# Kernel tuning notes

Hardware: AMD Instinct MI355X
Metric: run time of the kernel (lower is better)

The kernel has to match this reference:

```python
import jax, jax.numpy as jnp
import numpy as np

EMBED = 768
HEADS = 12
HEAD_DIM = EMBED // HEADS
FFN = 4 * EMBED
EPS = 1e-5


def setup_inputs() -> dict:
    key = jax.random.key(0)
    ks = jax.random.split(key, 12)
    s = 0.02
    inp = {
        'x': jax.random.normal(ks[0], (1, 4096, EMBED), dtype=jnp.float32),
        'Wq': jax.random.normal(ks[1], (EMBED, EMBED), dtype=jnp.float32) * s,
        'bq': jnp.zeros((EMBED,), jnp.float32),
        'Wk': jax.random.normal(ks[2], (EMBED, EMBED), dtype=jnp.float32) * s,
        'bk': jnp.zeros((EMBED,), jnp.float32),
        'Wv': jax.random.normal(ks[3], (EMBED, EMBED), dtype=jnp.float32) * s,
        'bv': jnp.zeros((EMBED,), jnp.float32),
        'Wo': jax.random.normal(ks[4], (EMBED, EMBED), dtype=jnp.float32) * s,
        'bo': jnp.zeros((EMBED,), jnp.float32),
        'ln1_g': jnp.ones((EMBED,), jnp.float32),
        'ln1_b': jnp.zeros((EMBED,), jnp.float32),
        'W1': jax.random.normal(ks[5], (EMBED, FFN), dtype=jnp.float32) * s,
        'b1': jnp.zeros((FFN,), jnp.float32),
        'W2': jax.random.normal(ks[6], (FFN, EMBED), dtype=jnp.float32) * s,
        'b2': jnp.zeros((EMBED,), jnp.float32),
        'ln2_g': jnp.ones((EMBED,), jnp.float32),
        'ln2_b': jnp.zeros((EMBED,), jnp.float32),
    }
    return inp


def _layernorm(x, g, b):
    mu = jnp.mean(x, axis=-1, keepdims=True)
    var = jnp.mean(jnp.square(x - mu), axis=-1, keepdims=True)
    return (x - mu) * jax.lax.rsqrt(var + EPS) * g + b


def reference(x, Wq, bq, Wk, bk, Wv, bv, Wo, bo, ln1_g, ln1_b, W1, b1, W2, b2, ln2_g, ln2_b):
    B, S, D = x.shape
    # QKV projections -> [B, H, S, d]
    def split_heads(t):
        return t.reshape(B, S, HEADS, HEAD_DIM).transpose(0, 2, 1, 3)
    q = split_heads(x @ Wq + bq)
    k = split_heads(x @ Wk + bk)
    v = split_heads(x @ Wv + bv)
    scores = jnp.einsum('bhqd,bhkd->bhqk', q, k) / np.sqrt(HEAD_DIM).astype(np.float32)
    attn = jax.nn.softmax(scores, axis=-1)
    ctx = jnp.einsum('bhqk,bhkd->bhqd', attn, v)
    ctx = ctx.transpose(0, 2, 1, 3).reshape(B, S, D)
    attn_out = ctx @ Wo + bo
    h = _layernorm(x + attn_out, ln1_g, ln1_b)
    ffn = jax.nn.gelu(h @ W1 + b1, approximate=False) @ W2 + b2
    return _layernorm(h + ffn, ln2_g, ln2_b)
```

## Files before the change

kernel.cpp:

```cpp
#include <hip/hip_runtime.h>
#include <hip/hip_bf16.h>

typedef __attribute__((ext_vector_type(8))) short s16x8;
typedef __attribute__((ext_vector_type(4))) int   i32x4;
typedef __attribute__((ext_vector_type(4))) float f32x4;
typedef __attribute__((ext_vector_type(8))) __bf16 bf16x8;

__device__ __forceinline__ short f2bf(float f) {
  unsigned u = __builtin_bit_cast(unsigned, f);
  u = (u + 0x7FFFu + ((u >> 16) & 1u)) >> 16;
  return (short)u;
}
__device__ __forceinline__ float bf2f(short s) {
  unsigned u = ((unsigned)(unsigned short)s) << 16;
  return __builtin_bit_cast(float, u);
}
__device__ __forceinline__ f32x4 mfma16(s16x8 a, s16x8 b, f32x4 c) {
  return __builtin_amdgcn_mfma_f32_16x16x32_bf16(
      __builtin_bit_cast(bf16x8, a), __builtin_bit_cast(bf16x8, b), c, 0, 0, 0);
}
__device__ __forceinline__ void gload16(const void* g, void* l) {
  __builtin_amdgcn_global_load_lds(
      (const __attribute__((address_space(1))) void*)g,
      (__attribute__((address_space(3))) void*)l, 16, 0, 0);
}

__global__ __launch_bounds__(256) void convert_x_kernel(const float* __restrict__ src,
                                                        short* __restrict__ dst, int n8) {
  int i = blockIdx.x * 256 + threadIdx.x;
  if (i >= n8) return;
  float4 v0 = ((const float4*)src)[i * 2];
  float4 v1 = ((const float4*)src)[i * 2 + 1];
  s16x8 o;
  o[0] = f2bf(v0.x); o[1] = f2bf(v0.y); o[2] = f2bf(v0.z); o[3] = f2bf(v0.w);
  o[4] = f2bf(v1.x); o[5] = f2bf(v1.y); o[6] = f2bf(v1.z); o[7] = f2bf(v1.w);
  *(s16x8*)&dst[i * 8] = o;
}

__global__ __launch_bounds__(256) void bconcat_kernel(const float* __restrict__ bq,
                                                      const float* __restrict__ bk,
                                                      const float* __restrict__ bv,
                                                      float* __restrict__ out) {
  int i = blockIdx.x * 256 + threadIdx.x;
  if (i < 2304) out[i] = i < 768 ? bq[i] : (i < 1536 ? bk[i - 768] : bv[i - 1536]);
}

__global__ __launch_bounds__(256) void wconv_kernel(const float* __restrict__ src,
                                                    short* __restrict__ dst, int K, int N) {
  __shared__ float t[32][33];
  int n0 = blockIdx.x * 32, k0 = blockIdx.y * 32;
  int tx = threadIdx.x & 31, ty = threadIdx.x >> 5;
#pragma unroll
  for (int r = 0; r < 4; ++r) t[ty + r * 8][tx] = src[(long)(k0 + ty + r * 8) * N + n0 + tx];
  __syncthreads();
#pragma unroll
  for (int r = 0; r < 4; ++r)
    dst[(long)(n0 + ty + r * 8) * K + k0 + tx] = f2bf(t[tx][ty + r * 8]);
}

__global__ __launch_bounds__(256) void vtrans_kernel(const short* __restrict__ qkv,
                                                     short* __restrict__ vt) {
  __shared__ short t[32][34];
  int c0 = blockIdx.x * 32, s0 = blockIdx.y * 32;
  int tx = threadIdx.x & 31, ty = threadIdx.x >> 5;
#pragma unroll
  for (int r = 0; r < 4; ++r)
    t[ty + r * 8][tx] = qkv[(long)(s0 + ty + r * 8) * 2304 + 1536 + c0 + tx];
  __syncthreads();
#pragma unroll
  for (int r = 0; r < 4; ++r)
    vt[(long)(c0 + ty + r * 8) * 4096 + s0 + tx] = t[tx][ty + r * 8];
}

template <int OUT_MODE>
__global__ __launch_bounds__(256) void gemm_kernel(const short* __restrict__ A,
                                                   const short* __restrict__ Bt,
                                                   const float* __restrict__ bias,
                                                   void* __restrict__ Cout,
                                                   int M, int N, int Kfull, int Ksub) {
  __shared__ short As[2][128 * 32];
  __shared__ short Bs[2][128 * 32];
  const int tid = threadIdx.x;
  const int wave = tid >> 6, lane = tid & 63;
  const int lr = lane & 15, lg = lane >> 4;
  const int wm = wave >> 1, wn = wave & 1;
  const int bm = blockIdx.x, bn = blockIdx.y;
  const long koff = (long)blockIdx.z * Ksub;

  f32x4 acc[4][4] = {};

  const int r0 = tid >> 2;
  const int cc = (tid & 3) * 8;
  const short* Ag0 = A + (long)(bm * 128 + r0) * Kfull + koff + cc;
  const short* Ag1 = Ag0 + (long)64 * Kfull;
  const short* Bg0 = Bt + (long)(bn * 128 + r0) * Kfull + koff + cc;
  const short* Bg1 = Bg0 + (long)64 * Kfull;

  auto STAGE = [&](int buf, int k0) {
    gload16(Ag0 + k0, &As[buf][tid * 8]);
    gload16(Ag1 + k0, &As[buf][64 * 32 + tid * 8]);
    gload16(Bg0 + k0, &Bs[buf][tid * 8]);
    gload16(Bg1 + k0, &Bs[buf][64 * 32 + tid * 8]);
  };
  auto COMPUTE = [&](int buf) {
    s16x8 af[4], bfr[4];
#pragma unroll
    for (int m = 0; m < 4; ++m) {
      int row = wm * 64 + m * 16 + lr;
      af[m] = *(const s16x8*)&As[buf][row * 32 + lg * 8];
    }
#pragma unroll
    for (int n = 0; n < 4; ++n) {
      int row = wn * 64 + n * 16 + lr;
      bfr[n] = *(const s16x8*)&Bs[buf][row * 32 + lg * 8];
    }
#pragma unroll
    for (int m = 0; m < 4; ++m)
#pragma unroll
      for (int n = 0; n < 4; ++n)
        acc[m][n] = mfma16(af[m], bfr[n], acc[m][n]);
  };

  const int nt = Ksub >> 5;
  STAGE(0, 0);
  int cur = 0;
  for (int t = 0; t < nt - 1; ++t) {
    STAGE(cur ^ 1, (t + 1) * 32);
    asm volatile("s_waitcnt vmcnt(4)" ::: "memory");
    __builtin_amdgcn_s_barrier();
    __builtin_amdgcn_sched_barrier(0);
    COMPUTE(cur);
    __builtin_amdgcn_s_barrier();
    cur ^= 1;
  }
  asm volatile("s_waitcnt vmcnt(0)" ::: "memory");
  __builtin_amdgcn_s_barrier();
  __builtin_amdgcn_sched_barrier(0);
  COMPUTE(cur);

  const int gr0 = bm * 128 + wm * 64 + lg * 4;
  const int gc0 = bn * 128 + wn * 64 + lr;
  float* outF = (float*)Cout + (long)blockIdx.z * M * N;
#pragma unroll
  for (int n = 0; n < 4; ++n) {
    int col = gc0 + n * 16;
    float bb = (blockIdx.z == 0) ? bias[col] : 0.f;
#pragma unroll
    for (int m = 0; m < 4; ++m) {
#pragma unroll
      for (int j = 0; j < 4; ++j) {
        int row = gr0 + m * 16 + j;
        float v = acc[m][n][j] + bb;
        if (OUT_MODE == 2) v = 0.5f * v * (1.0f + erff(v * 0.70710678118f));
        if (OUT_MODE == 1) outF[(long)row * N + col] = v;
        else ((short*)Cout)[(long)row * N + col] = f2bf(v);
      }
    }
  }
}

__global__ __launch_bounds__(256) void flash_kernel(const short* __restrict__ qkv,
                                                    const short* __restrict__ vt,
                                                    float* __restrict__ Opart,
                                                    float* __restrict__ Lpart) {
  __shared__ short Kt[2][64 * 64];
  __shared__ short Vs[2][64 * 64];
  __shared__ short Ps[128 * 72];
  const int tid = threadIdx.x;
  const int wave = tid >> 6, lane = tid & 63;
  const int lr = lane & 15, lg = lane >> 4;
  const int h = blockIdx.y, qb = blockIdx.x, sp = blockIdx.z;
  const int qc = h * 64;
  const int hc = 768 + h * 64;
  const int vr = h * 64;
  const float QSCALE = 0.125f * 1.44269504088896f;

  auto STAGEKV = [&](int buf, int s0) {
#pragma unroll
    for (int i = 0; i < 2; ++i) {
      int c = tid + i * 256;
      int row = c >> 3;
      int ch = (c & 7) ^ (row & 7);
      gload16(&qkv[(long)(s0 + row) * 2304 + hc + ch * 8], &Kt[buf][c * 8]);
      gload16(&vt[(long)(vr + row) * 4096 + s0 + ch * 8], &Vs[buf][c * 8]);
    }
  };

#pragma unroll
  for (int i = 0; i < 4; ++i) {
    int c = tid + i * 256;
    int row = c >> 3, cq = (c & 7) * 8;
    *(i32x4*)&Ps[row * 72 + cq] =
        *(const i32x4*)&qkv[(long)(qb * 128 + row) * 2304 + qc + cq];
  }
  STAGEKV(0, sp * 2048);
  __syncthreads();
  s16x8 qf[2][2];
#pragma unroll
  for (int m = 0; m < 2; ++m)
#pragma unroll
    for (int ks = 0; ks < 2; ++ks) {
      int row = wave * 32 + m * 16 + lr;
      s16x8 v = *(const s16x8*)&Ps[row * 72 + ks * 32 + lg * 8];
#pragma unroll
      for (int e = 0; e < 8; ++e) {
        __bf16 b = (__bf16)(bf2f(v[e]) * QSCALE);
        v[e] = (short)__builtin_bit_cast(unsigned short, b);
      }
      qf[m][ks] = v;
    }

  float l_part[8];
#pragma unroll
  for (int i = 0; i < 8; ++i) l_part[i] = 0.f;
  f32x4 oacc[2][4] = {};

  int cur = 0;
  for (int it = 0; it < 32; ++it) {
    if (it != 31) {
      STAGEKV(cur ^ 1, sp * 2048 + (it + 1) * 64);
      asm volatile("s_waitcnt vmcnt(4)" ::: "memory");
    } else {
      asm volatile("s_waitcnt vmcnt(0)" ::: "memory");
    }
    __builtin_amdgcn_s_barrier();
    __builtin_amdgcn_sched_barrier(0);

    f32x4 sacc[2][4] = {};
#pragma unroll
    for (int ks = 0; ks < 2; ++ks) {
      s16x8 kf[4];
#pragma unroll
      for (int n = 0; n < 4; ++n) {
        int row = n * 16 + lr;
        int chk = (ks * 4 + lg) ^ (lr & 7);
        kf[n] = *(const s16x8*)&Kt[cur][row * 64 + chk * 8];
      }
      __builtin_amdgcn_s_setprio(1);
#pragma unroll
      for (int m = 0; m < 2; ++m)
#pragma unroll
        for (int n = 0; n < 4; ++n)
          sacc[m][n] = mfma16(qf[m][ks], kf[n], sacc[m][n]);
      __builtin_amdgcn_s_setprio(0);
    }
#pragma unroll
    for (int m = 0; m < 2; ++m) {
#pragma unroll
      for (int j = 0; j < 4; ++j) {
        const int prow = wave * 32 + m * 16 + lg * 4 + j;
        float rs = 0.f;
#pragma unroll
        for (int n = 0; n < 4; ++n) {
          float p = __builtin_amdgcn_exp2f(sacc[m][n][j]);
          rs += p;
          ((__bf16*)Ps)[prow * 72 + n * 16 + lr] = (__bf16)p;
        }
        l_part[m * 4 + j] += rs;
      }
    }
#pragma unroll
    for (int ks = 0; ks < 2; ++ks) {
      s16x8 pf[2], vf[4];
#pragma unroll
      for (int m = 0; m < 2; ++m) {
        int row = wave * 32 + m * 16 + lr;
        pf[m] = *(const s16x8*)&Ps[row * 72 + ks * 32 + lg * 8];
      }
#pragma unroll
      for (int n = 0; n < 4; ++n) {
        int row = n * 16 + lr;
        int chk = (ks * 4 + lg) ^ (lr & 7);
        vf[n] = *(const s16x8*)&Vs[cur][row * 64 + chk * 8];
      }
      __builtin_amdgcn_s_setprio(1);
#pragma unroll
      for (int m = 0; m < 2; ++m)
#pragma unroll
        for (int n = 0; n < 4; ++n)
          oacc[m][n] = mfma16(pf[m], vf[n], oacc[m][n]);
      __builtin_amdgcn_s_setprio(0);
    }
    __builtin_amdgcn_s_barrier();
    cur ^= 1;
  }

  const long pbase = ((long)(h * 32 + qb) * 2 + sp) * 128;
#pragma unroll
  for (int m = 0; m < 2; ++m)
#pragma unroll
    for (int j = 0; j < 4; ++j) {
      float l = l_part[m * 4 + j];
      l += __shfl_xor(l, 1);
      l += __shfl_xor(l, 2);
      l += __shfl_xor(l, 4);
      l += __shfl_xor(l, 8);
      if (lr == 0) Lpart[pbase + wave * 32 + m * 16 + lg * 4 + j] = l;
    }
#pragma unroll
  for (int m = 0; m < 2; ++m)
#pragma unroll
    for (int n = 0; n < 4; ++n)
#pragma unroll
      for (int j = 0; j < 4; ++j) {
        int row = wave * 32 + m * 16 + lg * 4 + j;
        Opart[(pbase + row) * 64 + n * 16 + lr] = oacc[m][n][j];
      }
}

__global__ __launch_bounds__(256) void combine_kernel(const float* __restrict__ Opart,
                                                      const float* __restrict__ Lpart,
                                                      short* __restrict__ ctx) {
  const int row = blockIdx.x;
  const int col = blockIdx.y * 256 + threadIdx.x;
  const int h = col >> 6, c = col & 63;
  const int qb = row >> 7, r = row & 127;
  const long p0 = ((long)(h * 32 + qb) * 2) * 128 + r;
  const long p1 = p0 + 128;
  float l = Lpart[p0] + Lpart[p1];
  float o = Opart[p0 * 64 + c] + Opart[p1 * 64 + c];
  ctx[(long)row * 768 + col] = f2bf(o / l);
}

__global__ __launch_bounds__(256) void ln_kernel(const float* __restrict__ a,
                                                 const float* __restrict__ b,
                                                 const float* __restrict__ c,
                                                 const float* __restrict__ g,
                                                 const float* __restrict__ be,
                                                 float* __restrict__ of,
                                                 short* __restrict__ ob) {
  const int row = blockIdx.x;
  const int tid = threadIdx.x;
  const long base = (long)row * 768;
  float v[3];
  float s1 = 0.f, s2 = 0.f;
#pragma unroll
  for (int kk = 0; kk < 3; ++kk) {
    int i = tid + kk * 256;
    float x = a[base + i] + b[base + i] + c[base + i];
    v[kk] = x;
    s1 += x;
    s2 += x * x;
  }
#pragma unroll
  for (int off = 1; off < 64; off <<= 1) {
    s1 += __shfl_xor(s1, off);
    s2 += __shfl_xor(s2, off);
  }
  __shared__ float ws1[4], ws2[4];
  int wave = tid >> 6;
  if ((tid & 63) == 0) { ws1[wave] = s1; ws2[wave] = s2; }
  __syncthreads();
  s1 = ws1[0] + ws1[1] + ws1[2] + ws1[3];
  s2 = ws2[0] + ws2[1] + ws2[2] + ws2[3];
  float mean = s1 * (1.f / 768.f);
  float var = s2 * (1.f / 768.f) - mean * mean;
  float rstd = rsqrtf(var + 1e-5f);
#pragma unroll
  for (int kk = 0; kk < 3; ++kk) {
    int i = tid + kk * 256;
    float o = (v[kk] - mean) * rstd * g[i] + be[i];
    if (of) of[base + i] = o;
    if (ob) ob[base + i] = f2bf(o);
  }
}

extern "C" void kernel_launch(void* const* d_in, const int* in_sizes, int n_in,
                              void* d_out, int out_size, void* d_ws, size_t ws_size,
                              hipStream_t stream) {
  const float* x   = (const float*)d_in[0];
  const float* Wq  = (const float*)d_in[1];
  const float* bq  = (const float*)d_in[2];
  const float* Wk  = (const float*)d_in[3];
  const float* bk  = (const float*)d_in[4];
  const float* Wv  = (const float*)d_in[5];
  const float* bv  = (const float*)d_in[6];
  const float* Wo  = (const float*)d_in[7];
  const float* bo  = (const float*)d_in[8];
  const float* g1  = (const float*)d_in[9];
  const float* be1 = (const float*)d_in[10];
  const float* W1  = (const float*)d_in[11];
  const float* b1  = (const float*)d_in[12];
  const float* W2  = (const float*)d_in[13];
  const float* b2  = (const float*)d_in[14];
  const float* g2  = (const float*)d_in[15];
  const float* be2 = (const float*)d_in[16];

  char* ws = (char*)d_ws;
  size_t off = 0;
  auto alloc = [&](size_t bytes) {
    char* p = ws + off;
    off += (bytes + 255) & ~(size_t)255;
    return p;
  };
  short* xb     = (short*)alloc(4096ul * 768 * 2);
  short* wqkv_t = (short*)alloc(2304ul * 768 * 2);
  short* wo_t   = (short*)alloc(768ul * 768 * 2);
  short* w1_t   = (short*)alloc(3072ul * 768 * 2);
  short* w2_t   = (short*)alloc(768ul * 3072 * 2);
  float* bqkv   = (float*)alloc(2304ul * 4);
  short* qkv    = (short*)alloc(4096ul * 2304 * 2);
  short* vt     = (short*)alloc(768ul * 4096 * 2);
  short* ctx    = (short*)alloc(4096ul * 768 * 2);
  float* attn_o = (float*)alloc(4096ul * 768 * 4);
  short* h_b    = (short*)alloc(4096ul * 768 * 2);
  float* h_f    = (float*)alloc(4096ul * 768 * 4);
  short* f1     = (short*)alloc(4096ul * 3072 * 2);
  float* Opart  = (float*)f1;
  float* Lpart  = (float*)attn_o;
  float* attn_p = (float*)qkv;
  float* ffn_p  = (float*)qkv;

  convert_x_kernel<<<1536, 256, 0, stream>>>(x, xb, 4096 * 768 / 8);
  bconcat_kernel<<<9, 256, 0, stream>>>(bq, bk, bv, bqkv);
  wconv_kernel<<<dim3(24, 24), 256, 0, stream>>>(Wq, wqkv_t, 768, 768);
  wconv_kernel<<<dim3(24, 24), 256, 0, stream>>>(Wk, wqkv_t + 768 * 768, 768, 768);
  wconv_kernel<<<dim3(24, 24), 256, 0, stream>>>(Wv, wqkv_t + 2 * 768 * 768, 768, 768);
  wconv_kernel<<<dim3(24, 24), 256, 0, stream>>>(Wo, wo_t, 768, 768);
  wconv_kernel<<<dim3(96, 24), 256, 0, stream>>>(W1, w1_t, 768, 3072);
  wconv_kernel<<<dim3(24, 96), 256, 0, stream>>>(W2, w2_t, 3072, 768);

  gemm_kernel<0><<<dim3(32, 18), 256, 0, stream>>>(xb, wqkv_t, bqkv, qkv, 4096, 2304, 768, 768);
  vtrans_kernel<<<dim3(24, 128), 256, 0, stream>>>(qkv, vt);
  flash_kernel<<<dim3(32, 12, 2), 256, 0, stream>>>(qkv, vt, Opart, Lpart);
  combine_kernel<<<dim3(4096, 3), 256, 0, stream>>>(Opart, Lpart, ctx);
  gemm_kernel<1><<<dim3(32, 6, 2), 256, 0, stream>>>(ctx, wo_t, bo, attn_p, 4096, 768, 768, 384);
  ln_kernel<<<4096, 256, 0, stream>>>(x, attn_p, attn_p + 4096ul * 768, g1, be1, h_f, h_b);
  gemm_kernel<2><<<dim3(32, 24), 256, 0, stream>>>(h_b, w1_t, b1, f1, 4096, 3072, 768, 768);
  gemm_kernel<1><<<dim3(32, 6, 2), 256, 0, stream>>>(f1, w2_t, b2, ffn_p, 4096, 768, 3072, 1536);
  ln_kernel<<<4096, 256, 0, stream>>>(h_f, ffn_p, ffn_p + 4096ul * 768, g2, be2, (float*)d_out, nullptr);
}
```

Measured before the change: 264.0 us.

## Prefetch K/V tiles through registers into single LDS buffer and remap block order

The flash kernel's double-buffered direct global-to-LDS loads are replaced by register prefetch. The next K/V tile is loaded into registers while the current tile is computed, then written into a single swizzled LDS buffer at the top of each iteration. Halving the K/V shared memory is meant to improve occupancy. Block indices are also remapped so that consecutive hardware blocks are spread across heads and splits, which is meant to improve L2/XCD locality. The cost is extra VGPRs and a store-to-LDS step on the critical path at the start of each iteration.

```diff
diff --git a/kernel.cpp b/kernel.cpp
--- a/kernel.cpp
+++ b/kernel.cpp
@@ -163,28 +163,42 @@
                                                     const short* __restrict__ vt,
                                                     float* __restrict__ Opart,
                                                     float* __restrict__ Lpart) {
-  __shared__ short Kt[2][64 * 64];
-  __shared__ short Vs[2][64 * 64];
+  __shared__ short Kt[64 * 64];
+  __shared__ short Vs[64 * 64];
   __shared__ short Ps[128 * 72];
   const int tid = threadIdx.x;
   const int wave = tid >> 6, lane = tid & 63;
   const int lr = lane & 15, lg = lane >> 4;
-  const int h = blockIdx.y, qb = blockIdx.x, sp = blockIdx.z;
+  const int lb = blockIdx.x + 32 * blockIdx.y + 384 * blockIdx.z;
+  const int nlb = (lb & 7) * 96 + (lb >> 3);
+  const int qb = nlb & 31;
+  const int h = (nlb >> 5) % 12;
+  const int sp = nlb / 384;
   const int qc = h * 64;
   const int hc = 768 + h * 64;
   const int vr = h * 64;
   const float QSCALE = 0.125f * 1.44269504088896f;
 
-  auto STAGEKV = [&](int buf, int s0) {
+  i32x4 kr[2], vrg[2];
+  auto LOADREGS = [&](int s0) {
 #pragma unroll
     for (int i = 0; i < 2; ++i) {
-      int c = tid + i * 256;
-      int row = c >> 3;
-      int ch = (c & 7) ^ (row & 7);
-      gload16(&qkv[(long)(s0 + row) * 2304 + hc + ch * 8], &Kt[buf][c * 8]);
-      gload16(&vt[(long)(vr + row) * 4096 + s0 + ch * 8], &Vs[buf][c * 8]);
+      int c = tid + i * 256, row = c >> 3, ch = c & 7;
+      kr[i] = *(const i32x4*)&qkv[(long)(s0 + row) * 2304 + hc + ch * 8];
+      vrg[i] = *(const i32x4*)&vt[(long)(vr + row) * 4096 + s0 + ch * 8];
     }
   };
+  auto WRITELDS = [&]() {
+#pragma unroll
+    for (int i = 0; i < 2; ++i) {
+      int c = tid + i * 256, row = c >> 3, ch = c & 7;
+      int sc = ch ^ (row & 7);
+      *(i32x4*)&Kt[row * 64 + sc * 8] = kr[i];
+      *(i32x4*)&Vs[row * 64 + sc * 8] = vrg[i];
+    }
+  };
+
+  LOADREGS(sp * 2048);
 
 #pragma unroll
   for (int i = 0; i < 4; ++i) {
@@ -193,7 +207,6 @@
     *(i32x4*)&Ps[row * 72 + cq] =
         *(const i32x4*)&qkv[(long)(qb * 128 + row) * 2304 + qc + cq];
   }
-  STAGEKV(0, sp * 2048);
   __syncthreads();
   s16x8 qf[2][2];
 #pragma unroll
@@ -215,14 +228,10 @@
   for (int i = 0; i < 8; ++i) l_part[i] = 0.f;
   f32x4 oacc[2][4] = {};
 
-  int cur = 0;
   for (int it = 0; it < 32; ++it) {
-    if (it != 31) {
-      STAGEKV(cur ^ 1, sp * 2048 + (it + 1) * 64);
-      asm volatile("s_waitcnt vmcnt(4)" ::: "memory");
-    } else {
-      asm volatile("s_waitcnt vmcnt(0)" ::: "memory");
-    }
+    WRITELDS();
+    if (it != 31) LOADREGS(sp * 2048 + (it + 1) * 64);
+    asm volatile("s_waitcnt lgkmcnt(0)" ::: "memory");
     __builtin_amdgcn_s_barrier();
     __builtin_amdgcn_sched_barrier(0);
 
@@ -234,7 +243,7 @@
       for (int n = 0; n < 4; ++n) {
         int row = n * 16 + lr;
         int chk = (ks * 4 + lg) ^ (lr & 7);
-        kf[n] = *(const s16x8*)&Kt[cur][row * 64 + chk * 8];
+        kf[n] = *(const s16x8*)&Kt[row * 64 + chk * 8];
       }
       __builtin_amdgcn_s_setprio(1);
 #pragma unroll
@@ -271,7 +280,7 @@
       for (int n = 0; n < 4; ++n) {
         int row = n * 16 + lr;
         int chk = (ks * 4 + lg) ^ (lr & 7);
-        vf[n] = *(const s16x8*)&Vs[cur][row * 64 + chk * 8];
+        vf[n] = *(const s16x8*)&Vs[row * 64 + chk * 8];
       }
       __builtin_amdgcn_s_setprio(1);
 #pragma unroll
@@ -282,7 +291,6 @@
       __builtin_amdgcn_s_setprio(0);
     }
     __builtin_amdgcn_s_barrier();
-    cur ^= 1;
   }
 
   const long pbase = ((long)(h * 32 + qb) * 2 + sp) * 128;
```

After: 255.0 us. 3.4% less time.
